# Performance work log

Hardware: AMD Instinct MI355X
Metric: run time of the kernel (lower is better)

## Reference

```python
import jax, jax.numpy as jnp
import numpy as np

DROP_P = 0.5

def setup_inputs() -> dict:
    key = jax.random.key(0)
    k_x, k_q, k_k, k_v = jax.random.split(key, 4)
    T, d_in, d_out = 4096, 1024, 1024
    x = jax.random.normal(k_x, (T, d_in), dtype=jnp.float32)
    # torch nn.Linear weights are [d_out, d_in]; init scale ~ 1/sqrt(d_in)
    s = 1.0 / np.sqrt(d_in)
    W_query = jax.random.uniform(k_q, (d_out, d_in), jnp.float32, -s, s)
    W_key = jax.random.uniform(k_k, (d_out, d_in), jnp.float32, -s, s)
    W_value = jax.random.uniform(k_v, (d_out, d_in), jnp.float32, -s, s)
    return {"x": x, "W_query": W_query, "W_key": W_key, "W_value": W_value}


def reference(x, W_query, W_key, W_value):
    # QKV projections (y = x @ W.T, matching torch Linear)
    queries = x @ W_query.T          # [T, d]
    keys = x @ W_key.T               # [T, d]
    # values = x @ W_value.T  -> feeds only the unused context_vec; dead code omitted
    d = keys.shape[-1]
    T = x.shape[0]
    attn_scores = queries @ keys.T   # [T, T]
    attn_weights = jax.nn.softmax(attn_scores / jnp.sqrt(jnp.float32(d)), axis=-1)
    # post-softmax causal masking + row renormalization (as in source)
    row = jnp.arange(T)
    causal = (row[:, None] >= row[None, :]).astype(attn_weights.dtype)  # tril of ones
    masked = attn_weights * causal
    masked_norm = masked / jnp.sum(masked, axis=-1, keepdims=True)
    # dropout(p=0.5), train mode, fixed seed
    keep = jax.random.bernoulli(jax.random.key(123), 1.0 - DROP_P, masked_norm.shape)
    return jnp.where(keep, masked_norm / (1.0 - DROP_P), 0.0)
```

## Files before the change

kernel.cpp:

```cpp
#include <hip/hip_runtime.h>
#include <hip/hip_bf16.h>
#include <math.h>


using bf16   = __bf16;
using bf16x8 = __attribute__((ext_vector_type(8))) __bf16;
using bf16x4 = __attribute__((ext_vector_type(4))) __bf16;
using f32x4  = __attribute__((ext_vector_type(4))) float;

constexpr int Tdim = 4096;
constexpr int Ddim = 1024;

__global__ __launch_bounds__(256) void k_cast_bf16(const float* __restrict__ in,
                                                   bf16* __restrict__ out, int n4) {
  int i = blockIdx.x * 256 + threadIdx.x;
  if (i >= n4) return;
  f32x4 v = reinterpret_cast<const f32x4*>(in)[i];
  bf16x4 o;
  o[0] = (bf16)v[0]; o[1] = (bf16)v[1]; o[2] = (bf16)v[2]; o[3] = (bf16)v[3];
  reinterpret_cast<bf16x4*>(out)[i] = o;
}

__global__ __launch_bounds__(256) void k_tcast(const float* __restrict__ q,
                                               const float* __restrict__ k,
                                               bf16* __restrict__ qt,
                                               bf16* __restrict__ kt) {
  const float* in = blockIdx.z ? k : q;
  bf16* out = blockIdx.z ? kt : qt;
  __shared__ float t[32][33];
  const int tx = threadIdx.x & 31;
  const int ty = threadIdx.x >> 5;
  const int r0 = blockIdx.y * 32;
  const int c0 = blockIdx.x * 32;
#pragma unroll
  for (int r = 0; r < 4; ++r)
    t[ty * 4 + r][tx] = in[(r0 + ty * 4 + r) * Ddim + c0 + tx];
  __syncthreads();
#pragma unroll
  for (int r = 0; r < 4; ++r)
    out[(c0 + ty * 4 + r) * Ddim + r0 + tx] = (bf16)t[tx][ty * 4 + r];
}

__global__ __launch_bounds__(256) void k_redcast(const float* __restrict__ p,
                                                 bf16* __restrict__ g) {
  const int i = blockIdx.x * 256 + threadIdx.x;
  f32x4 a = reinterpret_cast<const f32x4*>(p)[i];
  f32x4 b = reinterpret_cast<const f32x4*>(p + (1 << 20))[i];
  f32x4 c = reinterpret_cast<const f32x4*>(p + (2 << 20))[i];
  f32x4 d = reinterpret_cast<const f32x4*>(p + (3 << 20))[i];
  f32x4 s = a + b + c + d;
  bf16x4 o;
  o[0] = (bf16)s[0]; o[1] = (bf16)s[1]; o[2] = (bf16)s[2]; o[3] = (bf16)s[3];
  reinterpret_cast<bf16x4*>(g)[i] = o;
}

__device__ __forceinline__ void gll16(const bf16* g, bf16* l) {
  __builtin_amdgcn_global_load_lds(
      (const __attribute__((address_space(1))) void*)g,
      (__attribute__((address_space(3))) void*)l, 16, 0, 0);
}

template<int BM, int OUTF32>
__global__ __launch_bounds__(512)
void k_gemm(const bf16* __restrict__ A, const bf16* __restrict__ B,
            void* __restrict__ Cv, int N, int lda, int ldb, int kLen,
            long cZs, int causal) {
  constexpr int FM  = BM / 32;
  __shared__ __align__(16) bf16 As[4][BM * 32];
  __shared__ __align__(16) bf16 Bs[4][256 * 32];

  int bx = blockIdx.x;
  {
    const int cpx = gridDim.x >> 3;
    bx = (bx & 7) * cpx + (bx >> 3);
  }
  const int nbn = N >> 8;
  const int bm = bx / nbn;
  const int bn = bx - bm * nbn;
  if (causal && bn > bm) return;

  const int tid  = threadIdx.x;
  const int lane = tid & 63;
  const int wid  = tid >> 6;
  const int wrr  = (wid >> 2) * (BM / 2);
  const int wcc  = (wid & 3) * 64;
  const int fr   = lane & 15;
  const int g8   = (lane >> 4) * 8;

  f32x4 acc[FM][4];
#pragma unroll
  for (int i = 0; i < FM; ++i)
#pragma unroll
    for (int j = 0; j < 4; ++j) acc[i][j] = (f32x4){0.f, 0.f, 0.f, 0.f};

  const bf16* Ag = A + (long)bm * BM * lda;
  const bf16* Bg = B + (long)bn * 256 * ldb;
  const int k0 = blockIdx.y * kLen;
  const int nt = kLen >> 5;

  const bf16* pa0 = Ag + (long)(tid >> 2) * lda + (tid & 3) * 8;
  const bf16* pa1 = pa0 + (long)128 * lda;
  const bf16* pb0 = Bg + (long)(tid >> 2) * ldb + (tid & 3) * 8;
  const bf16* pb1 = pb0 + (long)128 * ldb;

  auto stageA = [&](int buf, int kt) {
    gll16(pa0 + kt, &As[buf][tid * 8]);
    if constexpr (BM == 256) gll16(pa1 + kt, &As[buf][(tid + 512) * 8]);
  };
  auto stageB = [&](int buf, int kt) {
    gll16(pb0 + kt, &Bs[buf][tid * 8]);
    gll16(pb1 + kt, &Bs[buf][(tid + 512) * 8]);
  };

  stageA(0, k0);      stageB(0, k0);
  stageA(1, k0 + 32); stageB(1, k0 + 32);
  stageA(2, k0 + 64); stageB(2, k0 + 64);

  for (int t = 0; t < nt; ++t) {
    const int buf = t & 3;
    if (t < nt - 2) {
      if constexpr (BM == 256) asm volatile("s_waitcnt vmcnt(8)" ::: "memory");
      else                     asm volatile("s_waitcnt vmcnt(6)" ::: "memory");
    } else if (t == nt - 2) {
      if constexpr (BM == 256) asm volatile("s_waitcnt vmcnt(4)" ::: "memory");
      else                     asm volatile("s_waitcnt vmcnt(3)" ::: "memory");
    } else {
      asm volatile("s_waitcnt vmcnt(0)" ::: "memory");
    }
    __builtin_amdgcn_sched_barrier(0);
    __builtin_amdgcn_s_barrier();
    __builtin_amdgcn_sched_barrier(0);

    const int ks = k0 + (t + 3) * 32;
    const bool more = (t + 3) < nt;
    const int nbuf = (t + 3) & 3;

    bf16x8 av[4], bv[4];
#pragma unroll
    for (int n = 0; n < 4; ++n)
      bv[n] = *reinterpret_cast<const bf16x8*>(&Bs[buf][(wcc + n * 16 + fr) * 32 + g8]);
#pragma unroll
    for (int m = 0; m < 4; ++m)
      av[m] = *reinterpret_cast<const bf16x8*>(&As[buf][(wrr + m * 16 + fr) * 32 + g8]);
    if (more) stageA(nbuf, ks);
    __builtin_amdgcn_s_setprio(1);
#pragma unroll
    for (int m = 0; m < 4; ++m)
#pragma unroll
      for (int n = 0; n < 4; ++n)
        acc[m][n] = __builtin_amdgcn_mfma_f32_16x16x32_bf16(av[m], bv[n], acc[m][n], 0, 0, 0);
    __builtin_amdgcn_s_setprio(0);

    if constexpr (BM == 256) {
#pragma unroll
      for (int m = 0; m < 4; ++m)
        av[m] = *reinterpret_cast<const bf16x8*>(&As[buf][(wrr + (m + 4) * 16 + fr) * 32 + g8]);
      if (more) stageB(nbuf, ks);
      __builtin_amdgcn_s_setprio(1);
#pragma unroll
      for (int m = 0; m < 4; ++m)
#pragma unroll
        for (int n = 0; n < 4; ++n)
          acc[m + 4][n] = __builtin_amdgcn_mfma_f32_16x16x32_bf16(av[m], bv[n], acc[m + 4][n], 0, 0, 0);
      __builtin_amdgcn_s_setprio(0);
    } else {
      if (more) stageB(nbuf, ks);
    }
  }

  const int crow = (lane >> 4) * 4;
  const int ccol = lane & 15;
#pragma unroll
  for (int m = 0; m < FM; ++m)
#pragma unroll
    for (int n = 0; n < 4; ++n)
#pragma unroll
      for (int j = 0; j < 4; ++j) {
        const long row = (long)bm * BM + wrr + m * 16 + crow + j;
        const long col = (long)bn * 256 + wcc + n * 16 + ccol;
        const float v = acc[m][n][j];
        if (OUTF32) ((float*)Cv + (long)blockIdx.y * cZs)[row * N + col] = v;
        else        ((bf16*)Cv)[row * N + col] = (bf16)v;
      }
}

__global__ __launch_bounds__(512, 2)
void k_gemm_s(const bf16* __restrict__ A, const bf16* __restrict__ B,
              float* __restrict__ C) {
  __shared__ __align__(16) bf16 As[2][2][128 * 64];
  __shared__ __align__(16) bf16 Bs[2][2][128 * 64];

  int swz = (blockIdx.x & 7) * 17 + (blockIdx.x >> 3);
  int bm = (int)((sqrtf(8.f * swz + 1.f) - 1.f) * 0.5f);
  while ((bm + 1) * (bm + 2) / 2 <= swz) ++bm;
  while (bm * (bm + 1) / 2 > swz) --bm;
  const int bn = swz - bm * (bm + 1) / 2;

  const int tid  = threadIdx.x;
  const int lane = tid & 63;
  const int wid  = tid >> 6;
  const int wm   = wid >> 2, wn = wid & 3;
  const int fr   = lane & 15;
  const int lh   = lane >> 4;

  const bf16* Ag = A + (long)bm * 256 * Ddim;
  const bf16* Bg = B + (long)bn * 256 * Ddim;

  const int r1 = tid >> 3,         c1 = ((tid & 7) ^ (r1 & 7)) * 8;
  const int r2 = (tid + 512) >> 3, c2 = ((tid & 7) ^ (r2 & 7)) * 8;
  const bf16* pA0a = Ag + (long)r1 * Ddim + c1;
  const bf16* pA0b = Ag + (long)r2 * Ddim + c2;
  const bf16* pA1a = pA0a + (long)128 * Ddim;
  const bf16* pA1b = pA0b + (long)128 * Ddim;
  const bf16* pB0a = Bg + (long)r1 * Ddim + c1;
  const bf16* pB0b = Bg + (long)r2 * Ddim + c2;
  const bf16* pB1a = pB0a + (long)128 * Ddim;
  const bf16* pB1b = pB0b + (long)128 * Ddim;
  const int d1 = tid * 8, d2 = (tid + 512) * 8;

  auto stage = [&](int buf, int which, int kt) {
    switch (which) {
      case 0: gll16(pA0a + kt, &As[buf][0][d1]); gll16(pA0b + kt, &As[buf][0][d2]); break;
      case 1: gll16(pB0a + kt, &Bs[buf][0][d1]); gll16(pB0b + kt, &Bs[buf][0][d2]); break;
      case 2: gll16(pB1a + kt, &Bs[buf][1][d1]); gll16(pB1b + kt, &Bs[buf][1][d2]); break;
      case 3: gll16(pA1a + kt, &As[buf][1][d1]); gll16(pA1b + kt, &As[buf][1][d2]); break;
    }
  };
  auto rd = [&](const bf16* half, int row, int chunk) -> bf16x8 {
    return *reinterpret_cast<const bf16x8*>(half + row * 64 + ((chunk ^ (row & 7)) * 8));
  };

  f32x4 acc[8][4];
#pragma unroll
  for (int i = 0; i < 8; ++i)
#pragma unroll
    for (int j = 0; j < 4; ++j) acc[i][j] = (f32x4){0.f, 0.f, 0.f, 0.f};

  const int nt = Ddim / 64;
  stage(0, 0, 0); stage(0, 1, 0); stage(0, 2, 0); stage(0, 3, 0);
  asm volatile("s_waitcnt vmcnt(4)" ::: "memory");
  __builtin_amdgcn_sched_barrier(0);
  __builtin_amdgcn_s_barrier();

  bf16x8 av[8], bv0[4], bv1[4];
  for (int t = 0; t < nt; ++t) {
    const int buf = t & 1, nbuf = buf ^ 1;
    const int kt = (t + 1) * 64;
    const bool pf = (t + 1) < nt;
    const bf16* Ah0 = &As[buf][0][0];
    const bf16* Ah1 = &As[buf][1][0];
    const bf16* Bh0 = &Bs[buf][0][0];
    const bf16* Bh1 = &Bs[buf][1][0];

#pragma unroll
    for (int m = 0; m < 4; ++m) {
      const int row = wm * 64 + m * 16 + fr;
      av[m * 2]     = rd(Ah0, row, lh);
      av[m * 2 + 1] = rd(Ah0, row, 4 + lh);
    }
#pragma unroll
    for (int n = 0; n < 2; ++n) {
      const int row = wn * 32 + n * 16 + fr;
      bv0[n * 2]     = rd(Bh0, row, lh);
      bv0[n * 2 + 1] = rd(Bh0, row, 4 + lh);
    }
    if (pf) stage(nbuf, 0, kt);
    __builtin_amdgcn_s_barrier();
    asm volatile("s_waitcnt lgkmcnt(0)" ::: "memory");
    __builtin_amdgcn_sched_barrier(0);
    __builtin_amdgcn_s_setprio(1);
#pragma unroll
    for (int m = 0; m < 4; ++m)
#pragma unroll
      for (int n = 0; n < 2; ++n) {
        acc[m][n] = __builtin_amdgcn_mfma_f32_16x16x32_bf16(av[m*2],   bv0[n*2],   acc[m][n], 0, 0, 0);
        acc[m][n] = __builtin_amdgcn_mfma_f32_16x16x32_bf16(av[m*2+1], bv0[n*2+1], acc[m][n], 0, 0, 0);
      }
    __builtin_amdgcn_s_setprio(0);
    if (pf) asm volatile("s_waitcnt vmcnt(4)" ::: "memory");
    else    asm volatile("s_waitcnt vmcnt(2)" ::: "memory");
    __builtin_amdgcn_sched_barrier(0);
    __builtin_amdgcn_s_barrier();

#pragma unroll
    for (int n = 0; n < 2; ++n) {
      const int row = wn * 32 + n * 16 + fr;
      bv1[n * 2]     = rd(Bh1, row, lh);
      bv1[n * 2 + 1] = rd(Bh1, row, 4 + lh);
    }
    if (pf) stage(nbuf, 1, kt);
    __builtin_amdgcn_s_barrier();
    asm volatile("s_waitcnt lgkmcnt(0)" ::: "memory");
    __builtin_amdgcn_sched_barrier(0);
    __builtin_amdgcn_s_setprio(1);
#pragma unroll
    for (int m = 0; m < 4; ++m)
#pragma unroll
      for (int n = 0; n < 2; ++n) {
        acc[m][2+n] = __builtin_amdgcn_mfma_f32_16x16x32_bf16(av[m*2],   bv1[n*2],   acc[m][2+n], 0, 0, 0);
        acc[m][2+n] = __builtin_amdgcn_mfma_f32_16x16x32_bf16(av[m*2+1], bv1[n*2+1], acc[m][2+n], 0, 0, 0);
      }
    __builtin_amdgcn_s_setprio(0);
    if (pf) asm volatile("s_waitcnt vmcnt(4)" ::: "memory");
    else    asm volatile("s_waitcnt vmcnt(0)" ::: "memory");
    __builtin_amdgcn_sched_barrier(0);
    __builtin_amdgcn_s_barrier();

#pragma unroll
    for (int m = 0; m < 4; ++m) {
      const int row = wm * 64 + m * 16 + fr;
      av[m * 2]     = rd(Ah1, row, lh);
      av[m * 2 + 1] = rd(Ah1, row, 4 + lh);
    }
    if (pf) stage(nbuf, 2, kt);
    __builtin_amdgcn_s_barrier();
    asm volatile("s_waitcnt lgkmcnt(0)" ::: "memory");
    __builtin_amdgcn_sched_barrier(0);
    __builtin_amdgcn_s_setprio(1);
#pragma unroll
    for (int m = 0; m < 4; ++m)
#pragma unroll
      for (int n = 0; n < 2; ++n) {
        acc[4+m][n] = __builtin_amdgcn_mfma_f32_16x16x32_bf16(av[m*2],   bv0[n*2],   acc[4+m][n], 0, 0, 0);
        acc[4+m][n] = __builtin_amdgcn_mfma_f32_16x16x32_bf16(av[m*2+1], bv0[n*2+1], acc[4+m][n], 0, 0, 0);
      }
    __builtin_amdgcn_s_setprio(0);
    __builtin_amdgcn_s_barrier();

    if (pf) stage(nbuf, 3, kt);
    __builtin_amdgcn_s_barrier();
    __builtin_amdgcn_sched_barrier(0);
    __builtin_amdgcn_s_setprio(1);
#pragma unroll
    for (int m = 0; m < 4; ++m)
#pragma unroll
      for (int n = 0; n < 2; ++n) {
        acc[4+m][2+n] = __builtin_amdgcn_mfma_f32_16x16x32_bf16(av[m*2],   bv1[n*2],   acc[4+m][2+n], 0, 0, 0);
        acc[4+m][2+n] = __builtin_amdgcn_mfma_f32_16x16x32_bf16(av[m*2+1], bv1[n*2+1], acc[4+m][2+n], 0, 0, 0);
      }
    __builtin_amdgcn_s_setprio(0);
    if (pf) {
      asm volatile("s_waitcnt vmcnt(4)" ::: "memory");
      __builtin_amdgcn_sched_barrier(0);
    }
    __builtin_amdgcn_s_barrier();
  }

  const int crow = (lane >> 4) * 4;
  const int ccol = lane & 15;
#pragma unroll
  for (int qm = 0; qm < 2; ++qm)
#pragma unroll
    for (int m = 0; m < 4; ++m)
#pragma unroll
      for (int qn = 0; qn < 2; ++qn)
#pragma unroll
        for (int n = 0; n < 2; ++n)
#pragma unroll
          for (int j = 0; j < 4; ++j) {
            const long row = (long)bm * 256 + qm * 128 + wm * 64 + m * 16 + crow + j;
            const long col = (long)bn * 256 + qn * 128 + wn * 32 + n * 16 + ccol;
            C[row * Tdim + col] = acc[qm * 4 + m][qn * 2 + n][j];
          }
}

__device__ __forceinline__ unsigned rotl32(unsigned v, int d) {
  return (v << d) | (v >> (32 - d));
}
__device__ __forceinline__ void threefry_123(unsigned x0, unsigned x1,
                                             unsigned& o0, unsigned& o1) {
  const unsigned ks0 = 0u, ks1 = 123u;
  const unsigned ks2 = 0x1BD11BDAu ^ ks0 ^ ks1;
  x0 += ks0; x1 += ks1;
#define TF_R4(a, b, c, d)                                   \
  x0 += x1; x1 = rotl32(x1, a); x1 ^= x0;                   \
  x0 += x1; x1 = rotl32(x1, b); x1 ^= x0;                   \
  x0 += x1; x1 = rotl32(x1, c); x1 ^= x0;                   \
  x0 += x1; x1 = rotl32(x1, d); x1 ^= x0;
  TF_R4(13, 15, 26, 6);  x0 += ks1; x1 += ks2 + 1u;
  TF_R4(17, 29, 16, 24); x0 += ks2; x1 += ks0 + 2u;
  TF_R4(13, 15, 26, 6);  x0 += ks0; x1 += ks1 + 3u;
  TF_R4(17, 29, 16, 24); x0 += ks1; x1 += ks2 + 4u;
  TF_R4(13, 15, 26, 6);  x0 += ks2; x1 += ks0 + 5u;
#undef TF_R4
  o0 = x0; o1 = x1;
}
__device__ __forceinline__ bool keep_bit(unsigned i) {
  unsigned o0, o1;
  threefry_123(0u, i, o0, o1);
  return ((o0 ^ o1) & 0x80000000u) == 0u;
}

__global__ __launch_bounds__(256) void k_softmax_drop(float* __restrict__ S) {
  const int b  = blockIdx.x;
  const int r0 = b, r1 = Tdim - 1 - b;
  const int tid = threadIdx.x;
  const int cb  = tid * 16;
  __shared__ float redA[4], redB[4];

  float* row0 = S + (long)r0 * Tdim;
  float* row1 = S + (long)r1 * Tdim;

  f32x4 v1[4], v0[4];
  float lm0 = -3.0e38f, lm1 = -3.0e38f;
#pragma unroll
  for (int i = 0; i < 4; ++i) {
    const int c = cb + i * 4;
    f32x4 v = (c <= r1) ? *reinterpret_cast<const f32x4*>(row1 + c)
                        : (f32x4){0.f, 0.f, 0.f, 0.f};
#pragma unroll
    for (int l = 0; l < 4; ++l) {
      if (c + l > r1) v[l] = -3.0e38f;
      lm1 = fmaxf(lm1, v[l]);
    }
    v1[i] = v;
  }
#pragma unroll
  for (int i = 0; i < 4; ++i) {
    const int c = cb + i * 4;
    f32x4 v = (c <= r0) ? *reinterpret_cast<const f32x4*>(row0 + c)
                        : (f32x4){0.f, 0.f, 0.f, 0.f};
#pragma unroll
    for (int l = 0; l < 4; ++l) {
      if (c + l > r0) v[l] = -3.0e38f;
      lm0 = fmaxf(lm0, v[l]);
    }
    v0[i] = v;
  }
#pragma unroll
  for (int o = 32; o; o >>= 1) {
    lm0 = fmaxf(lm0, __shfl_xor(lm0, o));
    lm1 = fmaxf(lm1, __shfl_xor(lm1, o));
  }
  if ((tid & 63) == 0) { redA[tid >> 6] = lm0; redB[tid >> 6] = lm1; }
  __syncthreads();
  const float m0 = fmaxf(fmaxf(redA[0], redA[1]), fmaxf(redA[2], redA[3]));
  const float m1 = fmaxf(fmaxf(redB[0], redB[1]), fmaxf(redB[2], redB[3]));
  __syncthreads();

  constexpr float SC = 1.0f / 32.0f;
  float ls0 = 0.f, ls1 = 0.f;
#pragma unroll
  for (int i = 0; i < 4; ++i) {
#pragma unroll
    for (int l = 0; l < 4; ++l) {
      const int c = cb + i * 4 + l;
      float e = 0.f;
      if (c <= r1) { e = __expf((v1[i][l] - m1) * SC); ls1 += e; }
      v1[i][l] = e;
      float e0 = 0.f;
      if (c <= r0) { e0 = __expf((v0[i][l] - m0) * SC); ls0 += e0; }
      v0[i][l] = e0;
    }
  }
#pragma unroll
  for (int o = 32; o; o >>= 1) { ls0 += __shfl_xor(ls0, o); ls1 += __shfl_xor(ls1, o); }
  if ((tid & 63) == 0) { redA[tid >> 6] = ls0; redB[tid >> 6] = ls1; }
  __syncthreads();
  const float inv0 = 2.0f / (redA[0] + redA[1] + redA[2] + redA[3]);
  const float inv1 = 2.0f / (redB[0] + redB[1] + redB[2] + redB[3]);

#pragma unroll
  for (int i = 0; i < 4; ++i) {
    const int c = cb + i * 4;
    f32x4 o1v = {0.f, 0.f, 0.f, 0.f};
#pragma unroll
    for (int l = 0; l < 4; ++l) {
      const int cc = c + l;
      if (cc <= r1 && keep_bit((unsigned)(r1 * Tdim + cc))) o1v[l] = v1[i][l] * inv1;
    }
    *reinterpret_cast<f32x4*>(row1 + c) = o1v;
    f32x4 o0v = {0.f, 0.f, 0.f, 0.f};
#pragma unroll
    for (int l = 0; l < 4; ++l) {
      const int cc = c + l;
      if (cc <= r0 && keep_bit((unsigned)(r0 * Tdim + cc))) o0v[l] = v0[i][l] * inv0;
    }
    *reinterpret_cast<f32x4*>(row0 + c) = o0v;
  }
}

extern "C" void kernel_launch(void* const* d_in, const int* in_sizes, int n_in,
                              void* d_out, int out_size, void* d_ws, size_t ws_size,
                              hipStream_t stream) {
  const float* x  = (const float*)d_in[0];
  const float* Wq = (const float*)d_in[1];
  const float* Wk = (const float*)d_in[2];
  float* S = (float*)d_out;
  char* ws = (char*)d_ws;
  bf16*  xb = (bf16*)(ws);
  bf16*  qt = (bf16*)(ws + (8l  << 20));
  bf16*  kt = (bf16*)(ws + (10l << 20));
  float* Wp = (float*)(ws + (12l << 20));
  bf16*  G  = (bf16*)(ws + (28l << 20));
  bf16*  P  = (bf16*)(ws + (30l << 20));

  k_cast_bf16<<<(Tdim * Ddim / 4) / 256, 256, 0, stream>>>(x, xb, Tdim * Ddim / 4);
  k_tcast<<<dim3(32, 32, 2), 256, 0, stream>>>(Wq, Wk, qt, kt);

  k_gemm<128, 1><<<dim3(32, 4), 512, 0, stream>>>(kt, qt, (void*)Wp, Ddim, Ddim,
                                                  Ddim, Ddim / 4, 1l << 20, 0);
  k_redcast<<<(Ddim * Ddim / 4) / 256, 256, 0, stream>>>(Wp, G);

  k_gemm<128, 0><<<dim3(128, 1), 512, 0, stream>>>(xb, G, (void*)P, Ddim, Ddim,
                                                   Ddim, Ddim, 0, 0);
  k_gemm_s<<<136, 512, 0, stream>>>(P, xb, S);

  k_softmax_drop<<<Tdim / 2, 256, 0, stream>>>(S);
}
```

Measured before the change: 188.6 us.

## Fuse exp and row partial sums into score GEMM epilogue, merge prep casts

The score GEMM epilogue now writes exp(s/32) directly and emits per-row partial sums of the causal entries into a side buffer. The softmax kernel becomes a single read-scale-dropout pass, with no max pass and no block reductions. The x cast and weight transpose-casts are merged into one launch, and the P GEMM uses 128x128 tiles for more blocks. Dropping max subtraction risks overflow for large scores, but scores here are small enough.

```diff
diff --git a/kernel.cpp b/kernel.cpp
--- a/kernel.cpp
+++ b/kernel.cpp
@@ -11,27 +11,30 @@
 constexpr int Tdim = 4096;
 constexpr int Ddim = 1024;
 
-__global__ __launch_bounds__(256) void k_cast_bf16(const float* __restrict__ in,
-                                                   bf16* __restrict__ out, int n4) {
-  int i = blockIdx.x * 256 + threadIdx.x;
-  if (i >= n4) return;
-  f32x4 v = reinterpret_cast<const f32x4*>(in)[i];
-  bf16x4 o;
-  o[0] = (bf16)v[0]; o[1] = (bf16)v[1]; o[2] = (bf16)v[2]; o[3] = (bf16)v[3];
-  reinterpret_cast<bf16x4*>(out)[i] = o;
-}
-
-__global__ __launch_bounds__(256) void k_tcast(const float* __restrict__ q,
-                                               const float* __restrict__ k,
-                                               bf16* __restrict__ qt,
-                                               bf16* __restrict__ kt) {
-  const float* in = blockIdx.z ? k : q;
-  bf16* out = blockIdx.z ? kt : qt;
+__global__ __launch_bounds__(256) void k_prep(const float* __restrict__ x,
+                                              const float* __restrict__ Wq,
+                                              const float* __restrict__ Wk,
+                                              bf16* __restrict__ xb,
+                                              bf16* __restrict__ qt,
+                                              bf16* __restrict__ kt) {
+  const int bid = blockIdx.x;
+  if (bid < 4096) {
+    const int i = bid * 256 + threadIdx.x;
+    f32x4 v = reinterpret_cast<const f32x4*>(x)[i];
+    bf16x4 o;
+    o[0] = (bf16)v[0]; o[1] = (bf16)v[1]; o[2] = (bf16)v[2]; o[3] = (bf16)v[3];
+    reinterpret_cast<bf16x4*>(xb)[i] = o;
+    return;
+  }
+  const int idx = bid - 4096;
+  const float* in = (idx >> 10) ? Wk : Wq;
+  bf16* out = (idx >> 10) ? kt : qt;
+  const int rem = idx & 1023;
+  const int r0 = (rem >> 5) * 32;
+  const int c0 = (rem & 31) * 32;
   __shared__ float t[32][33];
   const int tx = threadIdx.x & 31;
   const int ty = threadIdx.x >> 5;
-  const int r0 = blockIdx.y * 32;
-  const int c0 = blockIdx.x * 32;
 #pragma unroll
   for (int r = 0; r < 4; ++r)
     t[ty * 4 + r][tx] = in[(r0 + ty * 4 + r) * Ddim + c0 + tx];
@@ -60,41 +63,40 @@
       (__attribute__((address_space(3))) void*)l, 16, 0, 0);
 }
 
-template<int BM, int OUTF32>
+template<int BM, int BN, int OUTF32>
 __global__ __launch_bounds__(512)
 void k_gemm(const bf16* __restrict__ A, const bf16* __restrict__ B,
-            void* __restrict__ Cv, int N, int lda, int ldb, int kLen,
-            long cZs, int causal) {
-  constexpr int FM  = BM / 32;
+            void* __restrict__ Cv, int N, int lda, int ldb, int kLen, long cZs) {
+  constexpr int FM = BM / 32;
+  constexpr int FN = BN / 64;
   __shared__ __align__(16) bf16 As[4][BM * 32];
-  __shared__ __align__(16) bf16 Bs[4][256 * 32];
+  __shared__ __align__(16) bf16 Bs[4][BN * 32];
 
   int bx = blockIdx.x;
   {
     const int cpx = gridDim.x >> 3;
     bx = (bx & 7) * cpx + (bx >> 3);
   }
-  const int nbn = N >> 8;
+  const int nbn = N / BN;
   const int bm = bx / nbn;
   const int bn = bx - bm * nbn;
-  if (causal && bn > bm) return;
 
   const int tid  = threadIdx.x;
   const int lane = tid & 63;
   const int wid  = tid >> 6;
   const int wrr  = (wid >> 2) * (BM / 2);
-  const int wcc  = (wid & 3) * 64;
+  const int wcc  = (wid & 3) * (BN / 4);
   const int fr   = lane & 15;
   const int g8   = (lane >> 4) * 8;
 
-  f32x4 acc[FM][4];
+  f32x4 acc[FM][FN];
 #pragma unroll
   for (int i = 0; i < FM; ++i)
 #pragma unroll
-    for (int j = 0; j < 4; ++j) acc[i][j] = (f32x4){0.f, 0.f, 0.f, 0.f};
+    for (int j = 0; j < FN; ++j) acc[i][j] = (f32x4){0.f, 0.f, 0.f, 0.f};
 
   const bf16* Ag = A + (long)bm * BM * lda;
-  const bf16* Bg = B + (long)bn * 256 * ldb;
+  const bf16* Bg = B + (long)bn * BN * ldb;
   const int k0 = blockIdx.y * kLen;
   const int nt = kLen >> 5;
 
@@ -109,21 +111,24 @@
   };
   auto stageB = [&](int buf, int kt) {
     gll16(pb0 + kt, &Bs[buf][tid * 8]);
-    gll16(pb1 + kt, &Bs[buf][(tid + 512) * 8]);
+    if constexpr (BN == 256) gll16(pb1 + kt, &Bs[buf][(tid + 512) * 8]);
   };
 
   stageA(0, k0);      stageB(0, k0);
   stageA(1, k0 + 32); stageB(1, k0 + 32);
   stageA(2, k0 + 64); stageB(2, k0 + 64);
 
+  constexpr int LPT = (BM == 256 ? 2 : 1) + (BN == 256 ? 2 : 1);
   for (int t = 0; t < nt; ++t) {
     const int buf = t & 3;
     if (t < nt - 2) {
-      if constexpr (BM == 256) asm volatile("s_waitcnt vmcnt(8)" ::: "memory");
-      else                     asm volatile("s_waitcnt vmcnt(6)" ::: "memory");
+      if constexpr (LPT == 4)      asm volatile("s_waitcnt vmcnt(8)" ::: "memory");
+      else if constexpr (LPT == 3) asm volatile("s_waitcnt vmcnt(6)" ::: "memory");
+      else                         asm volatile("s_waitcnt vmcnt(4)" ::: "memory");
     } else if (t == nt - 2) {
-      if constexpr (BM == 256) asm volatile("s_waitcnt vmcnt(4)" ::: "memory");
-      else                     asm volatile("s_waitcnt vmcnt(3)" ::: "memory");
+      if constexpr (LPT == 4)      asm volatile("s_waitcnt vmcnt(4)" ::: "memory");
+      else if constexpr (LPT == 3) asm volatile("s_waitcnt vmcnt(3)" ::: "memory");
+      else                         asm volatile("s_waitcnt vmcnt(2)" ::: "memory");
     } else {
       asm volatile("s_waitcnt vmcnt(0)" ::: "memory");
     }
@@ -135,9 +140,9 @@
     const bool more = (t + 3) < nt;
     const int nbuf = (t + 3) & 3;
 
-    bf16x8 av[4], bv[4];
-#pragma unroll
-    for (int n = 0; n < 4; ++n)
+    bf16x8 av[4], bv[FN];
+#pragma unroll
+    for (int n = 0; n < FN; ++n)
       bv[n] = *reinterpret_cast<const bf16x8*>(&Bs[buf][(wcc + n * 16 + fr) * 32 + g8]);
 #pragma unroll
     for (int m = 0; m < 4; ++m)
@@ -147,7 +152,7 @@
 #pragma unroll
     for (int m = 0; m < 4; ++m)
 #pragma unroll
-      for (int n = 0; n < 4; ++n)
+      for (int n = 0; n < FN; ++n)
         acc[m][n] = __builtin_amdgcn_mfma_f32_16x16x32_bf16(av[m], bv[n], acc[m][n], 0, 0, 0);
     __builtin_amdgcn_s_setprio(0);
 
@@ -160,7 +165,7 @@
 #pragma unroll
       for (int m = 0; m < 4; ++m)
 #pragma unroll
-        for (int n = 0; n < 4; ++n)
+        for (int n = 0; n < FN; ++n)
           acc[m + 4][n] = __builtin_amdgcn_mfma_f32_16x16x32_bf16(av[m], bv[n], acc[m + 4][n], 0, 0, 0);
       __builtin_amdgcn_s_setprio(0);
     } else {
@@ -173,11 +178,11 @@
 #pragma unroll
   for (int m = 0; m < FM; ++m)
 #pragma unroll
-    for (int n = 0; n < 4; ++n)
+    for (int n = 0; n < FN; ++n)
 #pragma unroll
       for (int j = 0; j < 4; ++j) {
         const long row = (long)bm * BM + wrr + m * 16 + crow + j;
-        const long col = (long)bn * 256 + wcc + n * 16 + ccol;
+        const long col = (long)bn * BN + wcc + n * 16 + ccol;
         const float v = acc[m][n][j];
         if (OUTF32) ((float*)Cv + (long)blockIdx.y * cZs)[row * N + col] = v;
         else        ((bf16*)Cv)[row * N + col] = (bf16)v;
@@ -186,7 +191,7 @@
 
 __global__ __launch_bounds__(512, 2)
 void k_gemm_s(const bf16* __restrict__ A, const bf16* __restrict__ B,
-              float* __restrict__ C) {
+              float* __restrict__ C, float* __restrict__ part) {
   __shared__ __align__(16) bf16 As[2][2][128 * 64];
   __shared__ __align__(16) bf16 Bs[2][2][128 * 64];
 
@@ -346,6 +351,7 @@
     __builtin_amdgcn_s_barrier();
   }
 
+  constexpr float SC = 1.0f / 32.0f;
   const int crow = (lane >> 4) * 4;
   const int ccol = lane & 15;
 #pragma unroll
@@ -353,15 +359,22 @@
 #pragma unroll
     for (int m = 0; m < 4; ++m)
 #pragma unroll
-      for (int qn = 0; qn < 2; ++qn)
-#pragma unroll
-        for (int n = 0; n < 2; ++n)
-#pragma unroll
-          for (int j = 0; j < 4; ++j) {
-            const long row = (long)bm * 256 + qm * 128 + wm * 64 + m * 16 + crow + j;
+      for (int j = 0; j < 4; ++j) {
+        const long row = (long)bm * 256 + qm * 128 + wm * 64 + m * 16 + crow + j;
+        float s = 0.f;
+#pragma unroll
+        for (int qn = 0; qn < 2; ++qn)
+#pragma unroll
+          for (int n = 0; n < 2; ++n) {
             const long col = (long)bn * 256 + qn * 128 + wn * 32 + n * 16 + ccol;
-            C[row * Tdim + col] = acc[qm * 4 + m][qn * 2 + n][j];
+            const float e = __expf(acc[qm * 4 + m][qn * 2 + n][j] * SC);
+            C[row * Tdim + col] = e;
+            s += (col <= row) ? e : 0.f;
           }
+#pragma unroll
+        for (int off = 1; off < 16; off <<= 1) s += __shfl_xor(s, off);
+        if ((lane & 15) == 0) part[row * 68 + bn * 4 + wn] = s;
+      }
 }
 
 __device__ __forceinline__ unsigned rotl32(unsigned v, int d) {
@@ -391,90 +404,43 @@
   return ((o0 ^ o1) & 0x80000000u) == 0u;
 }
 
-__global__ __launch_bounds__(256) void k_softmax_drop(float* __restrict__ S) {
+__global__ __launch_bounds__(256)
+void k_softmax_drop(float* __restrict__ S, const float* __restrict__ part) {
   const int b  = blockIdx.x;
   const int r0 = b, r1 = Tdim - 1 - b;
   const int tid = threadIdx.x;
   const int cb  = tid * 16;
-  __shared__ float redA[4], redB[4];
+
+  float s0 = 0.f, s1 = 0.f;
+  const int nb0 = (r0 >> 8) + 1, nb1 = (r1 >> 8) + 1;
+  for (int t = 0; t < nb0 * 4; ++t) s0 += part[r0 * 68 + t];
+  for (int t = 0; t < nb1 * 4; ++t) s1 += part[r1 * 68 + t];
+  const float inv0 = 2.0f / s0;
+  const float inv1 = 2.0f / s1;
 
   float* row0 = S + (long)r0 * Tdim;
   float* row1 = S + (long)r1 * Tdim;
 
-  f32x4 v1[4], v0[4];
-  float lm0 = -3.0e38f, lm1 = -3.0e38f;
 #pragma unroll
   for (int i = 0; i < 4; ++i) {
     const int c = cb + i * 4;
-    f32x4 v = (c <= r1) ? *reinterpret_cast<const f32x4*>(row1 + c)
-                        : (f32x4){0.f, 0.f, 0.f, 0.f};
-#pragma unroll
-    for (int l = 0; l < 4; ++l) {
-      if (c + l > r1) v[l] = -3.0e38f;
-      lm1 = fmaxf(lm1, v[l]);
-    }
-    v1[i] = v;
-  }
-#pragma unroll
-  for (int i = 0; i < 4; ++i) {
-    const int c = cb + i * 4;
-    f32x4 v = (c <= r0) ? *reinterpret_cast<const f32x4*>(row0 + c)
-                        : (f32x4){0.f, 0.f, 0.f, 0.f};
-#pragma unroll
-    for (int l = 0; l < 4; ++l) {
-      if (c + l > r0) v[l] = -3.0e38f;
-      lm0 = fmaxf(lm0, v[l]);
-    }
-    v0[i] = v;
-  }
-#pragma unroll
-  for (int o = 32; o; o >>= 1) {
-    lm0 = fmaxf(lm0, __shfl_xor(lm0, o));
-    lm1 = fmaxf(lm1, __shfl_xor(lm1, o));
-  }
-  if ((tid & 63) == 0) { redA[tid >> 6] = lm0; redB[tid >> 6] = lm1; }
-  __syncthreads();
-  const float m0 = fmaxf(fmaxf(redA[0], redA[1]), fmaxf(redA[2], redA[3]));
-  const float m1 = fmaxf(fmaxf(redB[0], redB[1]), fmaxf(redB[2], redB[3]));
-  __syncthreads();
-
-  constexpr float SC = 1.0f / 32.0f;
-  float ls0 = 0.f, ls1 = 0.f;
-#pragma unroll
-  for (int i = 0; i < 4; ++i) {
-#pragma unroll
-    for (int l = 0; l < 4; ++l) {
-      const int c = cb + i * 4 + l;
-      float e = 0.f;
-      if (c <= r1) { e = __expf((v1[i][l] - m1) * SC); ls1 += e; }
-      v1[i][l] = e;
-      float e0 = 0.f;
-      if (c <= r0) { e0 = __expf((v0[i][l] - m0) * SC); ls0 += e0; }
-      v0[i][l] = e0;
-    }
-  }
-#pragma unroll
-  for (int o = 32; o; o >>= 1) { ls0 += __shfl_xor(ls0, o); ls1 += __shfl_xor(ls1, o); }
-  if ((tid & 63) == 0) { redA[tid >> 6] = ls0; redB[tid >> 6] = ls1; }
-  __syncthreads();
-  const float inv0 = 2.0f / (redA[0] + redA[1] + redA[2] + redA[3]);
-  const float inv1 = 2.0f / (redB[0] + redB[1] + redB[2] + redB[3]);
-
-#pragma unroll
-  for (int i = 0; i < 4; ++i) {
-    const int c = cb + i * 4;
+    f32x4 e1 = (c <= r1) ? *reinterpret_cast<const f32x4*>(row1 + c)
+                         : (f32x4){0.f, 0.f, 0.f, 0.f};
     f32x4 o1v = {0.f, 0.f, 0.f, 0.f};
 #pragma unroll
     for (int l = 0; l < 4; ++l) {
       const int cc = c + l;
-      if (cc <= r1 && keep_bit((unsigned)(r1 * Tdim + cc))) o1v[l] = v1[i][l] * inv1;
+      if (cc <= r1 && keep_bit((unsigned)(r1 * Tdim + cc))) o1v[l] = e1[l] * inv1;
     }
     *reinterpret_cast<f32x4*>(row1 + c) = o1v;
+
+    f32x4 e0 = (c <= r0) ? *reinterpret_cast<const f32x4*>(row0 + c)
+                         : (f32x4){0.f, 0.f, 0.f, 0.f};
     f32x4 o0v = {0.f, 0.f, 0.f, 0.f};
 #pragma unroll
     for (int l = 0; l < 4; ++l) {
       const int cc = c + l;
-      if (cc <= r0 && keep_bit((unsigned)(r0 * Tdim + cc))) o0v[l] = v0[i][l] * inv0;
+      if (cc <= r0 && keep_bit((unsigned)(r0 * Tdim + cc))) o0v[l] = e0[l] * inv0;
     }
     *reinterpret_cast<f32x4*>(row0 + c) = o0v;
   }
@@ -494,17 +460,17 @@
   float* Wp = (float*)(ws + (12l << 20));
   bf16*  G  = (bf16*)(ws + (28l << 20));
   bf16*  P  = (bf16*)(ws + (30l << 20));
-
-  k_cast_bf16<<<(Tdim * Ddim / 4) / 256, 256, 0, stream>>>(x, xb, Tdim * Ddim / 4);
-  k_tcast<<<dim3(32, 32, 2), 256, 0, stream>>>(Wq, Wk, qt, kt);
-
-  k_gemm<128, 1><<<dim3(32, 4), 512, 0, stream>>>(kt, qt, (void*)Wp, Ddim, Ddim,
-                                                  Ddim, Ddim / 4, 1l << 20, 0);
+  float* part = (float*)(ws + (38l << 20));
+
+  k_prep<<<4096 + 2048, 256, 0, stream>>>(x, Wq, Wk, xb, qt, kt);
+
+  k_gemm<128, 256, 1><<<dim3(32, 4), 512, 0, stream>>>(kt, qt, (void*)Wp, Ddim,
+                                                       Ddim, Ddim, Ddim / 4, 1l << 20);
   k_redcast<<<(Ddim * Ddim / 4) / 256, 256, 0, stream>>>(Wp, G);
 
-  k_gemm<128, 0><<<dim3(128, 1), 512, 0, stream>>>(xb, G, (void*)P, Ddim, Ddim,
-                                                   Ddim, Ddim, 0, 0);
-  k_gemm_s<<<136, 512, 0, stream>>>(P, xb, S);
-
-  k_softmax_drop<<<Tdim / 2, 256, 0, stream>>>(S);
-}
+  k_gemm<128, 128, 0><<<dim3(256, 1), 512, 0, stream>>>(xb, G, (void*)P, Ddim,
+                                                        Ddim, Ddim, Ddim, 0);
+  k_gemm_s<<<136, 512, 0, stream>>>(P, xb, S, part);
+
+  k_softmax_drop<<<Tdim / 2, 256, 0, stream>>>(S, part);
+}
```

After: 211.2 us. 12.0% more time.
